# Optimization experiments

Measured on AMD Instinct MI355X. Metric: run time of the kernel, lower is better.

The kernel has to match this reference:

```python
import jax, jax.numpy as jnp
import numpy as np

B_GR = 128    # graphs per batch
N0 = 512      # nodes per graph before pooling
E_PER = 4096  # edges per graph (kept static; pooled-away edges get weight 0)
H = 128       # hidden
F = 128       # num_features (== hidden)
C = 10        # num_classes
K_HOP = 3     # Jacobi polynomial order (hop_num)
A_J, B_J = 1.0, 1.0
EPS = 1e-5


def _bn(h, g, b):
    # training-mode BatchNorm1d: batch stats, biased variance
    m = jnp.mean(h, 0)
    v = jnp.mean((h - m) ** 2, 0)
    return (h - m) * jax.lax.rsqrt(v + EPS) * g + b


def _forward(x, convW, convb, bnW, bnB, bn7W, bn7B, attW, theta,
             lin1W, lin1b, lin2W, lin2b, lin3W, lin3b, src, dst):
    w = jnp.ones((src.shape[0],), x.dtype)  # edge weights; 0 => filtered edge
    n = N0
    h = x
    reads = []
    for i in range(5):
        N = B_GR * n
        # symmetric GCN normalization with self loops on the weighted graph
        deg = jax.ops.segment_sum(w, dst, num_segments=N) + 1.0
        dinv = jax.lax.rsqrt(deg)
        enorm = dinv[src] * dinv[dst] * w   # per-edge norm [E]
        snorm = dinv * dinv                 # self-loop norm [N]
        prop = lambda m_: jax.ops.segment_sum(enorm[:, None] * m_[src], dst, num_segments=N) + m_ * snorm[:, None]
        pvec = lambda v_: jax.ops.segment_sum(enorm * v_[src], dst, num_segments=N) + v_ * snorm
        # GCNConv -> BN -> ReLU
        h = prop(h @ convW[i]) + convb[i]
        h = jax.nn.relu(_bn(h, bnW[i], bnB[i]))
        # JacobiPool: Jacobi-polynomial diffusion of attention scores
        s0 = h @ attW[i]                    # [N]
        polys = [s0, 0.5 * ((A_J - B_J) * s0 + (A_J + B_J + 2.0) * pvec(s0))]
        for kk in range(2, K_HOP + 1):
            c0 = 2 * kk * (kk + A_J + B_J) * (2 * kk + A_J + B_J - 2)
            c1 = (2 * kk + A_J + B_J - 1) * (2 * kk + A_J + B_J) * (2 * kk + A_J + B_J - 2)
            c2 = (2 * kk + A_J + B_J - 1) * (A_J * A_J - B_J * B_J)
            c3 = 2 * (kk + A_J - 1) * (kk + B_J - 1) * (2 * kk + A_J + B_J)
            polys.append((c1 * pvec(polys[-1]) + c2 * polys[-1] - c3 * polys[-2]) / c0)
        score = sum(theta[i, j] * polys[j] for j in range(K_HOP + 1))
        # top-k node selection per graph (ratio 0.5 -> static k)
        k = n // 2
        _, idx = jax.lax.top_k(score.reshape(B_GR, n), k)
        sel = (idx + (jnp.arange(B_GR) * n)[:, None]).reshape(-1)  # global node ids [B*k]
        h = h[sel] * jnp.tanh(score[sel])[:, None]
        # remap/filter edges to surviving nodes (masked, static edge count)
        new_id = jnp.full((N,), -1, jnp.int32).at[sel].set(jnp.arange(B_GR * k, dtype=jnp.int32))
        ns, nd = new_id[src], new_id[dst]
        valid = (ns >= 0) & (nd >= 0) & (w > 0)
        w = valid.astype(x.dtype)
        src = jnp.where(valid, ns, 0)
        dst = jnp.where(valid, nd, 0)
        # readout: global max pool || global mean pool per graph
        xg = h.reshape(B_GR, k, H)
        reads.append(jnp.concatenate([xg.max(1), xg.mean(1)], -1))
        n = k
    g = sum(reads) / 5.0                    # [B, 2H]
    g = jax.nn.relu(_bn(g @ lin1W + lin1b, bnW[5], bnB[5]))
    g = jax.nn.relu(_bn(g @ lin2W + lin2b, bn7W, bn7B))
    return jax.nn.log_softmax(g @ lin3W + lin3b, -1)


def setup_inputs() -> dict:
    key = jax.random.key(0)
    ks = jax.random.split(key, 8)
    N = B_GR * N0
    E = B_GR * E_PER
    rng = np.random.default_rng(0)
    off = np.repeat(np.arange(B_GR, dtype=np.int32) * N0, E_PER)
    src = jnp.asarray(off + rng.integers(0, N0, E).astype(np.int32))
    dst = jnp.asarray(off + rng.integers(0, N0, E).astype(np.int32))
    s = 1.0 / np.sqrt(H)
    return {
        "x": jax.random.normal(ks[0], (N, F), jnp.float32),
        "convW": jax.random.normal(ks[1], (5, H, H), jnp.float32) * s,
        "convb": jnp.zeros((5, H), jnp.float32),
        "bnW": jnp.ones((6, H), jnp.float32),
        "bnB": jnp.zeros((6, H), jnp.float32),
        "bn7W": jnp.ones((H // 2,), jnp.float32),
        "bn7B": jnp.zeros((H // 2,), jnp.float32),
        "attW": jax.random.normal(ks[2], (5, H), jnp.float32) * s,
        "theta": jax.random.normal(ks[3], (5, K_HOP + 1), jnp.float32) * 0.5,
        "lin1W": jax.random.normal(ks[4], (2 * H, H), jnp.float32) * (1.0 / np.sqrt(2 * H)),
        "lin1b": jnp.zeros((H,), jnp.float32),
        "lin2W": jax.random.normal(ks[5], (H, H // 2), jnp.float32) * s,
        "lin2b": jnp.zeros((H // 2,), jnp.float32),
        "lin3W": jax.random.normal(ks[6], (H // 2, C), jnp.float32) * (1.0 / np.sqrt(H // 2)),
        "lin3b": jnp.zeros((C,), jnp.float32),
        "src": src,
        "dst": dst,
    }


def reference(x, convW, convb, bnW, bnB, bn7W, bn7B, attW, theta,
              lin1W, lin1b, lin2W, lin2b, lin3W, lin3b, src, dst):
    return _forward(x, convW, convb, bnW, bnB, bn7W, bn7B, attW, theta,
                    lin1W, lin1b, lin2W, lin2b, lin3W, lin3b, src, dst)
```

## Files before the change

kernel.cpp:

```cpp
#include <hip/hip_runtime.h>
#include <hip/hip_bf16.h>

#define B_GRAPH 128
#define ETOT    (128*4096)
#define N0G     (128*512)
#define HF      128
#define STSZ    2048

union IGSmem {
    float Ws[64*HF];
    struct { int cnt4[4][512]; int cur[512]; float dvl[512]; } ini;
};

__global__ __launch_bounds__(256) void k_init_gemm(
    const float* __restrict__ A, const float* __restrict__ Wg, float* __restrict__ C,
    const int* __restrict__ s_in, const int* __restrict__ d_in_,
    int* __restrict__ srcw, int* __restrict__ dstw, float* __restrict__ wv,
    int2* __restrict__ csr, int2* __restrict__ rb2, float* __restrict__ dinvv,
    float* __restrict__ gacc, float* __restrict__ statsH,
    float* __restrict__ st0, float* __restrict__ st1, float* __restrict__ st2)
{
    __shared__ IGSmem sm;
    int t = threadIdx.x;
    if (blockIdx.x >= 128){
        int tx = t & 15, ty = t >> 4;
        int r0 = (blockIdx.x - 128)*128 + ty*8, c0 = tx*4;
        float acc[8][8];
        #pragma unroll
        for (int j=0;j<8;++j)
            #pragma unroll
            for (int l=0;l<8;++l) acc[j][l] = 0.f;
        for (int kh = 0; kh < 2; ++kh){
            __syncthreads();
            {
                float4* d4 = (float4*)sm.Ws;
                const float4* s4 = (const float4*)(Wg + kh*64*HF);
                #pragma unroll
                for (int i2 = 0; i2 < 8; ++i2) d4[t + i2*256] = s4[t + i2*256];
            }
            __syncthreads();
            for (int k4 = 0; k4 < 16; ++k4){
                float4 av[8];
                #pragma unroll
                for (int j=0;j<8;++j)
                    av[j] = *(const float4*)(A + (size_t)(r0+j)*HF + kh*64 + k4*4);
                #pragma unroll
                for (int kk=0; kk<4; ++kk){
                    int kl = k4*4 + kk;
                    float4 w0 = *(const float4*)(sm.Ws + kl*HF + c0);
                    float4 w1 = *(const float4*)(sm.Ws + kl*HF + c0 + 64);
                    #pragma unroll
                    for (int j=0;j<8;++j){
                        float a = reinterpret_cast<const float*>(&av[j])[kk];
                        acc[j][0] += a*w0.x; acc[j][1] += a*w0.y; acc[j][2] += a*w0.z; acc[j][3] += a*w0.w;
                        acc[j][4] += a*w1.x; acc[j][5] += a*w1.y; acc[j][6] += a*w1.z; acc[j][7] += a*w1.w;
                    }
                }
            }
        }
        #pragma unroll
        for (int j=0;j<8;++j){
            *(float4*)(C + (size_t)(r0+j)*HF + c0)      = make_float4(acc[j][0],acc[j][1],acc[j][2],acc[j][3]);
            *(float4*)(C + (size_t)(r0+j)*HF + c0 + 64) = make_float4(acc[j][4],acc[j][5],acc[j][6],acc[j][7]);
        }
    } else {
        int g = blockIdx.x;
        int wid = t >> 6;
        for (int l = t; l < 2048; l += 256) ((int*)sm.ini.cnt4)[l] = 0;
        gacc[g*256 + t] = 0.f;
        if (g == 0){
            if (t < 256){ statsH[t] = 0.f; if (t < 128) statsH[256+t] = 0.f; }
            for (int i = t; i < STSZ; i += 256){ st0[i] = 0.f; st1[i] = 0.f; st2[i] = 0.f; }
        }
        __syncthreads();
        for (int j = t; j < 4096; j += 256){
            int e = g*4096 + j;
            int sg = s_in[e], dg = d_in_[e];
            srcw[e] = sg; dstw[e] = dg; wv[e] = 1.f;
            atomicAdd(&sm.ini.cnt4[wid][dg & 511], 1);
        }
        __syncthreads();
        int c0 = sm.ini.cnt4[0][2*t] + sm.ini.cnt4[1][2*t] + sm.ini.cnt4[2][2*t] + sm.ini.cnt4[3][2*t];
        int c1 = sm.ini.cnt4[0][2*t+1] + sm.ini.cnt4[1][2*t+1] + sm.ini.cnt4[2][2*t+1] + sm.ini.cnt4[3][2*t+1];
        int pairsum = c0 + c1;
        sm.ini.cur[t] = pairsum;
        __syncthreads();
        for (int off = 1; off < 256; off <<= 1){
            int a = (t >= off) ? sm.ini.cur[t-off] : 0;
            __syncthreads();
            sm.ini.cur[t] += a;
            __syncthreads();
        }
        int begpair = sm.ini.cur[t] - pairsum;
        __syncthreads();
        sm.ini.cur[2*t]   = begpair;
        sm.ini.cur[2*t+1] = begpair + c0;
        sm.ini.cnt4[0][2*t]   = c0;
        sm.ini.cnt4[0][2*t+1] = c1;
        __syncthreads();
        for (int l = t; l < 512; l += 256){
            int cl = sm.ini.cnt4[0][l];
            rb2[g*512 + l] = make_int2(g*4096 + sm.ini.cur[l], cl);
            float dv = rsqrtf((float)cl + 1.f);
            sm.ini.dvl[l] = dv;
            dinvv[g*512 + l] = dv;
        }
        __syncthreads();
        for (int j = t; j < 4096; j += 256){
            int e = g*4096 + j;
            int sg = srcw[e], dl = dstw[e] & 511;
            int p = atomicAdd(&sm.ini.cur[dl], 1);
            csr[g*4096 + p] = make_int2(sg, __float_as_int(sm.ini.dvl[sg & 511]));
        }
    }
}

__global__ __launch_bounds__(256) void k_prop_stats(const float* __restrict__ Y, const float* __restrict__ cb,
                                                    const int2* __restrict__ rb2, const int2* __restrict__ cp,
                                                    const float* __restrict__ dinv,
                                                    float* __restrict__ X, float* __restrict__ st,
                                                    int n, int lb, int Nn){
    __shared__ float rs[1024], rq[1024];
    int xcd = blockIdx.x & 7, c = blockIdx.x >> 3;
    int g = xcd*16 + (c >> lb);
    int m = c & ((1 << lb) - 1);
    int nd = threadIdx.x >> 5;
    int v = g*n + m*8 + nd;
    int f4 = threadIdx.x & 31;
    float dv = dinv[v];
    float4 y = *(const float4*)(Y + (size_t)v*HF + f4*4);
    float4 acc = make_float4(0.f, 0.f, 0.f, 0.f);
    int2 rb = rb2[v];
    int e0 = rb.x, e1 = rb.x + rb.y;
    for (int j = e0; j < e1; ++j){
        int2 e = cp[j];
        int s = e.x & (Nn - 1);
        float en = __int_as_float(e.y);
        float4 h = *(const float4*)(Y + (size_t)s*HF + f4*4);
        acc.x += en*h.x; acc.y += en*h.y; acc.z += en*h.z; acc.w += en*h.w;
    }
    int f = f4*4;
    acc.x = y.x*dv*dv + dv*acc.x + cb[f];
    acc.y = y.y*dv*dv + dv*acc.y + cb[f+1];
    acc.z = y.z*dv*dv + dv*acc.z + cb[f+2];
    acc.w = y.w*dv*dv + dv*acc.w + cb[f+3];
    *(float4*)(X + (size_t)v*HF + f) = acc;
    *(float4*)&rs[nd*HF + f] = acc;
    *(float4*)&rq[nd*HF + f] = make_float4(acc.x*acc.x, acc.y*acc.y, acc.z*acc.z, acc.w*acc.w);
    __syncthreads();
    if (threadIdx.x < 128){
        int tt = threadIdx.x;
        float s = 0.f, q = 0.f;
        #pragma unroll
        for (int j = 0; j < 8; ++j){ s += rs[j*HF + tt]; q += rq[j*HF + tt]; }
        atomicAdd(&st[xcd*256 + tt], s);
        atomicAdd(&st[xcd*256 + 128 + tt], q);
    }
}

__global__ __launch_bounds__(256) void k_gemm(const float* __restrict__ A, const float* __restrict__ Wg,
                                              float* __restrict__ C)
{
    __shared__ float Ws[64*HF];
    int t = threadIdx.x;
    int tx = t & 15, ty = t >> 4;
    int r0 = blockIdx.x*128 + ty*8, c0 = tx*4;
    float acc[8][8];
    #pragma unroll
    for (int j=0;j<8;++j)
        #pragma unroll
        for (int l=0;l<8;++l) acc[j][l] = 0.f;
    for (int kh = 0; kh < 2; ++kh){
        __syncthreads();
        {
            float4* d4 = (float4*)Ws;
            const float4* s4 = (const float4*)(Wg + kh*64*HF);
            #pragma unroll
            for (int i2 = 0; i2 < 8; ++i2) d4[t + i2*256] = s4[t + i2*256];
        }
        __syncthreads();
        for (int k4 = 0; k4 < 16; ++k4){
            float4 av[8];
            #pragma unroll
            for (int j=0;j<8;++j)
                av[j] = *(const float4*)(A + (size_t)(r0+j)*HF + kh*64 + k4*4);
            #pragma unroll
            for (int kk=0; kk<4; ++kk){
                int kl = k4*4 + kk;
                float4 w0 = *(const float4*)(Ws + kl*HF + c0);
                float4 w1 = *(const float4*)(Ws + kl*HF + c0 + 64);
                #pragma unroll
                for (int j=0;j<8;++j){
                    float a = reinterpret_cast<const float*>(&av[j])[kk];
                    acc[j][0] += a*w0.x; acc[j][1] += a*w0.y; acc[j][2] += a*w0.z; acc[j][3] += a*w0.w;
                    acc[j][4] += a*w1.x; acc[j][5] += a*w1.y; acc[j][6] += a*w1.z; acc[j][7] += a*w1.w;
                }
            }
        }
    }
    #pragma unroll
    for (int j=0;j<8;++j){
        *(float4*)(C + (size_t)(r0+j)*HF + c0)      = make_float4(acc[j][0],acc[j][1],acc[j][2],acc[j][3]);
        *(float4*)(C + (size_t)(r0+j)*HF + c0 + 64) = make_float4(acc[j][4],acc[j][5],acc[j][6],acc[j][7]);
    }
}

struct __align__(16) KSmem {
    struct {
        int2  eds[4096]; int2 rbl[512];
        float dvv[512], p0[512], p1[512], p2[512];
        float ss[512]; int si[512]; float tss[256]; int nid[512];
        int   cntN[256], curN[256]; float dvn[256];
        float bna[128], bnb[128]; float red[1024]; float awl[128];
    } gr;
};

__global__ __launch_bounds__(1024) void k_graph(
    const float* __restrict__ H, const float* __restrict__ stats,
    const float* __restrict__ gw, const float* __restrict__ gb,
    const float* __restrict__ aw, const float* __restrict__ th,
    const int2* __restrict__ rb2, int2* __restrict__ csr, const float* __restrict__ dinv,
    int* __restrict__ srcw, int* __restrict__ dstw, float* __restrict__ wv,
    float* __restrict__ P, float* __restrict__ gacc,
    int2* __restrict__ rb2n, float* __restrict__ dinvn,
    float* __restrict__ stZero,
    const float* __restrict__ lin1W, const float* __restrict__ lin1b,
    float* __restrict__ t1g, float* __restrict__ statsH,
    float invN, float ca2, float cc2, float ca3, float cc3,
    int n, int last)
{
    int g = blockIdx.x, t = threadIdx.x;
    int k = n >> 1;
    __shared__ KSmem sm;

    if (t < 256) stZero[(g & 7)*256 + t] = 0.f;
    if (t < 128){
        float s = 0.f, q = 0.f;
        #pragma unroll
        for (int b2 = 0; b2 < 8; ++b2){ s += stats[b2*256 + t]; q += stats[b2*256 + 128 + t]; }
        float mean = s*invN;
        float var  = q*invN - mean*mean;
        float iv   = rsqrtf(var + 1e-5f);
        sm.gr.bna[t] = iv*gw[t];
        sm.gr.bnb[t] = gb[t] - mean*iv*gw[t];
        sm.gr.awl[t] = aw[t];
    }
    for (int l = t; l < n; l += 1024){
        int2 rb = rb2[g*n + l];
        sm.gr.rbl[l] = make_int2(rb.x - g*4096, rb.y);
        sm.gr.dvv[l] = dinv[g*n + l];
    }
    __syncthreads();
    int medg = sm.gr.rbl[n-1].x + sm.gr.rbl[n-1].y;
    for (int j = t; j < medg; j += 1024){
        int2 e = csr[g*4096 + j];
        sm.gr.eds[j] = make_int2(e.x & (n-1), e.y);
    }
    {
        int l = t >> 1, h = t & 1;
        float part = 0.f;
        if (l < n){
            const float* hp = H + ((size_t)g*n + l)*HF + h*64;
            #pragma unroll
            for (int j = 0; j < 16; ++j){
                float4 v = *(const float4*)(hp + j*4);
                int f = h*64 + j*4;
                float4 a4 = *(const float4*)&sm.gr.bna[f];
                float4 b4 = *(const float4*)&sm.gr.bnb[f];
                float4 w4 = *(const float4*)&sm.gr.awl[f];
                part += fmaxf(v.x*a4.x + b4.x, 0.f)*w4.x
                      + fmaxf(v.y*a4.y + b4.y, 0.f)*w4.y
                      + fmaxf(v.z*a4.z + b4.z, 0.f)*w4.z
                      + fmaxf(v.w*a4.w + b4.w, 0.f)*w4.w;
            }
        }
        sm.gr.red[t] = part;
    }
    __syncthreads();
    for (int l = t; l < n; l += 1024) sm.gr.p0[l] = sm.gr.red[2*l] + sm.gr.red[2*l+1];
    __syncthreads();
    for (int l = t; l < n; l += 1024){
        int2 rc = sm.gr.rbl[l];
        float acc = 0.f;
        for (int j = 0; j < rc.y; ++j){
            int2 e = sm.gr.eds[rc.x + j];
            acc += __int_as_float(e.y) * sm.gr.p0[e.x];
        }
        float dv = sm.gr.dvv[l];
        sm.gr.p1[l] = 2.f*(sm.gr.p0[l]*dv*dv + dv*acc);
    }
    __syncthreads();
    for (int l = t; l < n; l += 1024){
        int2 rc = sm.gr.rbl[l];
        float acc = 0.f;
        for (int j = 0; j < rc.y; ++j){
            int2 e = sm.gr.eds[rc.x + j];
            acc += __int_as_float(e.y) * sm.gr.p1[e.x];
        }
        float dv = sm.gr.dvv[l];
        sm.gr.p2[l] = ca2*(sm.gr.p1[l]*dv*dv + dv*acc) + cc2*sm.gr.p0[l];
    }
    __syncthreads();
    float t0v = th[0], t1v = th[1], t2c = th[2], t3v = th[3];
    for (int l = t; l < n; l += 1024){
        int2 rc = sm.gr.rbl[l];
        float acc = 0.f;
        for (int j = 0; j < rc.y; ++j){
            int2 e = sm.gr.eds[rc.x + j];
            acc += __int_as_float(e.y) * sm.gr.p2[e.x];
        }
        float dv = sm.gr.dvv[l];
        float tv = sm.gr.p2[l]*dv*dv + dv*acc;
        float p3 = ca3*tv + cc3*sm.gr.p1[l];
        sm.gr.ss[l] = t0v*sm.gr.p0[l] + t1v*sm.gr.p1[l] + t2c*sm.gr.p2[l] + t3v*p3;
    }
    __syncthreads();
    for (int l = t; l < n; l += 1024){
        float sl = sm.gr.ss[l];
        int r = 0;
        for (int j = 0; j < n; j += 4){
            float4 s4 = *(const float4*)&sm.gr.ss[j];
            r += (s4.x > sl) || (s4.x == sl && (j    ) < l);
            r += (s4.y > sl) || (s4.y == sl && (j + 1) < l);
            r += (s4.z > sl) || (s4.z == sl && (j + 2) < l);
            r += (s4.w > sl) || (s4.w == sl && (j + 3) < l);
        }
        if (r < k){
            sm.gr.nid[l] = r;
            sm.gr.si[r]  = l;
            sm.gr.tss[r] = tanhf(sl);
        } else {
            sm.gr.nid[l] = -1;
        }
    }
    __syncthreads();
    {
        int f4 = t & 31, rl = t >> 5;
        int f = f4*4;
        float4 a4 = *(const float4*)&sm.gr.bna[f];
        float4 b4 = *(const float4*)&sm.gr.bnb[f];
        float4 mx = make_float4(-3.4e38f,-3.4e38f,-3.4e38f,-3.4e38f);
        float4 smv = make_float4(0.f,0.f,0.f,0.f);
        for (int r = rl; r < k; r += 32){
            int old = sm.gr.si[r];
            float4 hv = *(const float4*)(H + ((size_t)g*n + old)*HF + f);
            float ts = sm.gr.tss[r];
            float4 v;
            v.x = fmaxf(hv.x*a4.x + b4.x, 0.f)*ts;
            v.y = fmaxf(hv.y*a4.y + b4.y, 0.f)*ts;
            v.z = fmaxf(hv.z*a4.z + b4.z, 0.f)*ts;
            v.w = fmaxf(hv.w*a4.w + b4.w, 0.f)*ts;
            *(float4*)(P + ((size_t)g*k + r)*HF + f) = v;
            mx.x = fmaxf(mx.x, v.x); mx.y = fmaxf(mx.y, v.y);
            mx.z = fmaxf(mx.z, v.z); mx.w = fmaxf(mx.w, v.w);
            smv.x += v.x; smv.y += v.y; smv.z += v.z; smv.w += v.w;
        }
        float* scr = (float*)sm.gr.eds;
        *(float4*)&scr[rl*128 + f]        = mx;
        *(float4*)&scr[4096 + rl*128 + f] = smv;
        __syncthreads();
        if (t < 128){
            float m = -3.4e38f, s = 0.f;
            #pragma unroll
            for (int j = 0; j < 32; ++j){
                m = fmaxf(m, scr[j*128 + t]);
                s += scr[4096 + j*128 + t];
            }
            gacc[g*256 + t] += m;
            gacc[g*256 + 128 + t] += s / (float)k;
        }
    }
    if (last){
        __syncthreads();
        int c = t & 127, h = t >> 7;
        float s = 0.f;
        int k0 = h*32;
        #pragma unroll
        for (int kk = 0; kk < 32; ++kk)
            s += gacc[g*256 + k0 + kk] * lin1W[(k0 + kk)*128 + c];
        sm.gr.red[t] = s;
        __syncthreads();
        if (t < 512) sm.gr.red[t] += sm.gr.red[t+512];
        __syncthreads();
        if (t < 256) sm.gr.red[t] += sm.gr.red[t+256];
        __syncthreads();
        if (t < 128){
            float v = (sm.gr.red[t] + sm.gr.red[t+128]) * 0.2f + lin1b[t];
            t1g[g*128 + t] = v;
            atomicAdd(&statsH[t], v);
            atomicAdd(&statsH[128+t], v*v);
        }
        return;
    }
    __syncthreads();
    if (t < k) sm.gr.cntN[t] = 0;
    __syncthreads();
    for (int j = t; j < 4096; j += 1024){
        int e = g*4096 + j;
        float we = wv[e];
        int valid = 0, ns = 0, nd = 0;
        if (we > 0.5f){
            int sl = srcw[e] & (n-1);
            int dl = dstw[e] & (n-1);
            ns = sm.gr.nid[sl]; nd = sm.gr.nid[dl];
            valid = (ns >= 0) && (nd >= 0);
        }
        if (valid){
            srcw[e] = g*k + ns; dstw[e] = g*k + nd; wv[e] = 1.f;
            atomicAdd(&sm.gr.cntN[nd], 1);
        } else {
            srcw[e] = 0; dstw[e] = 0; wv[e] = 0.f;
        }
    }
    __syncthreads();
    int c = (t < 256) ? ((t < k) ? sm.gr.cntN[t] : 0) : 0;
    if (t < 256) sm.gr.si[t] = c;
    __syncthreads();
    for (int off = 1; off < 256; off <<= 1){
        int a = 0;
        if (t < 256 && t >= off) a = sm.gr.si[t-off];
        __syncthreads();
        if (t < 256) sm.gr.si[t] += a;
        __syncthreads();
    }
    if (t < k){
        int beg = sm.gr.si[t] - c;
        rb2n[g*k + t] = make_int2(g*4096 + beg, c);
        float dv = rsqrtf((float)c + 1.f);
        dinvn[g*k + t] = dv;
        sm.gr.dvn[t] = dv;
        sm.gr.curN[t] = beg;
    }
    __syncthreads();
    for (int j = t; j < 4096; j += 1024){
        int e = g*4096 + j;
        if (wv[e] > 0.5f){
            int sg = srcw[e], dl = dstw[e] & (k-1);
            int p = atomicAdd(&sm.gr.curN[dl], 1);
            csr[g*4096 + p] = make_int2(sg, __float_as_int(sm.gr.dvn[sg & (k-1)]));
        }
    }
}

__global__ __launch_bounds__(128) void k_head2(const float* __restrict__ t1, const float* __restrict__ gw,
                                               const float* __restrict__ gb, const float* __restrict__ W2,
                                               const float* __restrict__ b2, float* __restrict__ sh,
                                               float* __restrict__ t2){
    int r = blockIdx.x, t = threadIdx.x;
    int cc = t & 63, h = t >> 6;
    __shared__ float row[128];
    __shared__ float red[128];
    {
        float mean = sh[t] * (1.f/128.f);
        float var  = sh[128+t]*(1.f/128.f) - mean*mean;
        float iv   = rsqrtf(var + 1e-5f);
        float v = (t1[r*128+t] - mean)*iv*gw[t] + gb[t];
        row[t] = fmaxf(v, 0.f);
    }
    __syncthreads();
    float s = 0.f;
    #pragma unroll
    for (int kk = 0; kk < 64; ++kk)
        s += row[h*64+kk] * W2[(h*64+kk)*64 + cc];
    red[t] = s;
    __syncthreads();
    if (h == 0){
        float v = red[cc] + red[cc+64] + b2[cc];
        t2[r*64+cc] = v;
        atomicAdd(&sh[256+cc], v);
        atomicAdd(&sh[320+cc], v*v);
    }
}
__global__ __launch_bounds__(64) void k_head3(const float* __restrict__ t2, const float* __restrict__ gw,
                                              const float* __restrict__ gb, const float* __restrict__ W3,
                                              const float* __restrict__ b3, const float* __restrict__ sh,
                                              float* __restrict__ out){
    int r = blockIdx.x, t = threadIdx.x;
    float mean = sh[256+t]*(1.f/128.f);
    float var  = sh[320+t]*(1.f/128.f) - mean*mean;
    float iv   = rsqrtf(var + 1e-5f);
    float v = fmaxf((t2[r*64+t]-mean)*iv*gw[t] + gb[t], 0.f);
    float lg[10];
    #pragma unroll
    for (int j = 0; j < 10; ++j){
        float p = v * W3[t*10 + j];
        for (int off = 32; off; off >>= 1) p += __shfl_down(p, off);
        lg[j] = p;
    }
    if (t == 0){
        float m = -3.4e38f;
        #pragma unroll
        for (int j = 0; j < 10; ++j){ lg[j] += b3[j]; m = fmaxf(m, lg[j]); }
        float se = 0.f;
        #pragma unroll
        for (int j = 0; j < 10; ++j) se += expf(lg[j] - m);
        float l = logf(se) + m;
        #pragma unroll
        for (int j = 0; j < 10; ++j) out[r*10 + j] = lg[j] - l;
    }
}

extern "C" void kernel_launch(void* const* d_in, const int* in_sizes, int n_in,
                              void* d_out, int out_size, void* d_ws, size_t ws_size,
                              hipStream_t stream){
    const float* x     = (const float*)d_in[0];
    const float* convW = (const float*)d_in[1];
    const float* convb = (const float*)d_in[2];
    const float* bnW   = (const float*)d_in[3];
    const float* bnB   = (const float*)d_in[4];
    const float* bn7W  = (const float*)d_in[5];
    const float* bn7B  = (const float*)d_in[6];
    const float* attW  = (const float*)d_in[7];
    const float* theta = (const float*)d_in[8];
    const float* lin1W = (const float*)d_in[9];
    const float* lin1b = (const float*)d_in[10];
    const float* lin2W = (const float*)d_in[11];
    const float* lin2b = (const float*)d_in[12];
    const float* lin3W = (const float*)d_in[13];
    const float* lin3b = (const float*)d_in[14];
    const int*   src0  = (const int*)d_in[15];
    const int*   dst0  = (const int*)d_in[16];

    char* base = (char*)d_ws;
    size_t off = 0;
    auto take = [&](size_t bytes) -> void* {
        void* p = base + off;
        off = (off + bytes + 255) & ~(size_t)255;
        return p;
    };
    float* bufGP = (float*)take((size_t)N0G*HF*4);
    float* bufHA = (float*)take((size_t)N0G*HF*4);
    float* bufHB = (float*)take((size_t)(N0G/2)*HF*4);
    int*   srcw  = (int*)  take((size_t)ETOT*4);
    int*   dstw  = (int*)  take((size_t)ETOT*4);
    float* w     = (float*)take((size_t)ETOT*4);
    int2*  csr_p = (int2*) take((size_t)ETOT*8);
    int2*  rb2A  = (int2*) take((size_t)N0G*8);
    int2*  rb2B  = (int2*) take((size_t)N0G*8);
    float* dinvA = (float*)take((size_t)N0G*4);
    float* dinvB = (float*)take((size_t)N0G*4);
    float* st[3];
    st[0] = (float*)take(STSZ*4);
    st[1] = (float*)take(STSZ*4);
    st[2] = (float*)take(STSZ*4);
    float* gacc  = (float*)take((size_t)B_GRAPH*256*4);
    float* t1    = (float*)take((size_t)B_GRAPH*128*4);
    float* t2    = (float*)take((size_t)B_GRAPH*64*4);
    float* statsH= (float*)take(384*4);

    auto coef = [](int kk, float& ca, float& cc){
        double a = 1.0, b = 1.0;
        double c0 = 2.0*kk*(kk+a+b)*(2.0*kk+a+b-2.0);
        double c1 = (2.0*kk+a+b-1.0)*(2.0*kk+a+b)*(2.0*kk+a+b-2.0);
        double c3 = 2.0*(kk+a-1.0)*(kk+b-1.0)*(2.0*kk+a+b);
        ca = (float)(c1/c0); cc = (float)(-c3/c0);
    };
    float ca2, cc2, ca3, cc3;
    coef(2, ca2, cc2);
    coef(3, ca3, cc3);

    k_init_gemm<<<128 + 512, 256, 0, stream>>>(x, convW, bufGP,
                                               src0, dst0, srcw, dstw, w, csr_p, rb2A, dinvA,
                                               gacc, statsH, st[0], st[1], st[2]);
    k_prop_stats<<<N0G/8, 256, 0, stream>>>(bufGP, convb, rb2A, csr_p, dinvA, bufHA, st[0], 512, 6, N0G);

    float* G = bufGP + (size_t)4*1024*1024;

    for (int i = 0; i < 5; ++i){
        int n = 512 >> i;
        int kk = n >> 1;
        int Nn = B_GRAPH*n;
        int2*  rb_cur = (i & 1) ? rb2B : rb2A;
        int2*  rb_nxt = (i & 1) ? rb2A : rb2B;
        float* dv_cur = (i & 1) ? dinvB : dinvA;
        float* dv_nxt = (i & 1) ? dinvA : dinvB;
        float* Hcur = (i & 1) ? bufHB : bufHA;
        float* Hnxt = (i & 1) ? bufHA : bufHB;

        k_graph<<<B_GRAPH, 1024, 0, stream>>>(Hcur, st[i % 3], bnW + i*HF, bnB + i*HF, attW + i*HF,
                                              theta + i*4, rb_cur, csr_p, dv_cur,
                                              srcw, dstw, w, bufGP, gacc, rb_nxt, dv_nxt,
                                              st[(i + 1) % 3],
                                              lin1W, lin1b, t1, statsH,
                                              1.0f/(float)Nn, ca2, cc2, ca3, cc3, n, (i == 4) ? 1 : 0);
        if (i < 4){
            int wnext = i + 1;
            int rows = B_GRAPH * kk;
            k_gemm<<<rows/128, 256, 0, stream>>>(bufGP, convW + (size_t)wnext*HF*HF, G);
            int lbn = (kk == 256) ? 5 : (kk == 128) ? 4 : (kk == 64) ? 3 : 2;
            k_prop_stats<<<rows/8, 256, 0, stream>>>(G, convb + wnext*HF, rb_nxt, csr_p, dv_nxt,
                                                     Hnxt, st[(i + 1) % 3], kk, lbn, rows);
        }
    }

    k_head2<<<B_GRAPH, 128, 0, stream>>>(t1, bnW + 5*HF, bnB + 5*HF, lin2W, lin2b, statsH, t2);
    k_head3<<<B_GRAPH, 64, 0, stream>>>(t2, bn7W, bn7B, lin3W, lin3b, statsH, (float*)d_out);
}
```

Baseline: 410.7 us.

## Split score kernel out, fuse BN/ReLU/gather into GEMM, rebuild CSR per-node

Moves the attention-score dot product out of the per-graph pool kernel into a wide grid-parallel k_score kernel. The pooled feature matrix is no longer written; instead the next GEMM gathers the selected rows, applies BN+ReLU+tanh scaling on load, and multiplies. The edge arrays (src/dst/weight) are dropped, and the next-level CSR is built directly from the current CSR using the kept-node map, avoiding a scan over all 4096 edges with atomics. Clamping masks are added on CSR indices and lengths, and there is one extra launch per level.

```diff
diff --git a/kernel.cpp b/kernel.cpp
--- a/kernel.cpp
+++ b/kernel.cpp
@@ -15,7 +15,6 @@
 __global__ __launch_bounds__(256) void k_init_gemm(
     const float* __restrict__ A, const float* __restrict__ Wg, float* __restrict__ C,
     const int* __restrict__ s_in, const int* __restrict__ d_in_,
-    int* __restrict__ srcw, int* __restrict__ dstw, float* __restrict__ wv,
     int2* __restrict__ csr, int2* __restrict__ rb2, float* __restrict__ dinvv,
     float* __restrict__ gacc, float* __restrict__ statsH,
     float* __restrict__ st0, float* __restrict__ st1, float* __restrict__ st2)
@@ -75,9 +74,7 @@
         __syncthreads();
         for (int j = t; j < 4096; j += 256){
             int e = g*4096 + j;
-            int sg = s_in[e], dg = d_in_[e];
-            srcw[e] = sg; dstw[e] = dg; wv[e] = 1.f;
-            atomicAdd(&sm.ini.cnt4[wid][dg & 511], 1);
+            atomicAdd(&sm.ini.cnt4[wid][d_in_[e] & 511], 1);
         }
         __syncthreads();
         int c0 = sm.ini.cnt4[0][2*t] + sm.ini.cnt4[1][2*t] + sm.ini.cnt4[2][2*t] + sm.ini.cnt4[3][2*t];
@@ -108,9 +105,9 @@
         __syncthreads();
         for (int j = t; j < 4096; j += 256){
             int e = g*4096 + j;
-            int sg = srcw[e], dl = dstw[e] & 511;
+            int sg = s_in[e], dl = d_in_[e] & 511;
             int p = atomicAdd(&sm.ini.cur[dl], 1);
-            csr[g*4096 + p] = make_int2(sg, __float_as_int(sm.ini.dvl[sg & 511]));
+            csr[g*4096 + (p & 4095)] = make_int2(sg, __float_as_int(sm.ini.dvl[sg & 511]));
         }
     }
 }
@@ -131,7 +128,8 @@
     float4 y = *(const float4*)(Y + (size_t)v*HF + f4*4);
     float4 acc = make_float4(0.f, 0.f, 0.f, 0.f);
     int2 rb = rb2[v];
-    int e0 = rb.x, e1 = rb.x + rb.y;
+    int len = min(max(rb.y, 0), 4096);
+    int e0 = rb.x, e1 = rb.x + len;
     for (int j = e0; j < e1; ++j){
         int2 e = cp[j];
         int s = e.x & (Nn - 1);
@@ -158,13 +156,77 @@
     }
 }
 
-__global__ __launch_bounds__(256) void k_gemm(const float* __restrict__ A, const float* __restrict__ Wg,
-                                              float* __restrict__ C)
+__global__ __launch_bounds__(256) void k_score(
+    const float* __restrict__ H, const float* __restrict__ stats,
+    const float* __restrict__ gw, const float* __restrict__ gb,
+    const float* __restrict__ aw, float* __restrict__ s0G, float invN)
+{
+    __shared__ float bna[128], bnb[128], awl[128];
+    int t = threadIdx.x;
+    if (t < 128){
+        float s = 0.f, q = 0.f;
+        #pragma unroll
+        for (int b2 = 0; b2 < 8; ++b2){ s += stats[b2*256 + t]; q += stats[b2*256 + 128 + t]; }
+        float mean = s*invN;
+        float var  = q*invN - mean*mean;
+        float iv   = rsqrtf(var + 1e-5f);
+        bna[t] = iv*gw[t];
+        bnb[t] = gb[t] - mean*iv*gw[t];
+        awl[t] = aw[t];
+    }
+    __syncthreads();
+    int v = blockIdx.x*128 + (t >> 1);
+    int h = t & 1;
+    const float* hp = H + (size_t)v*HF + h*64;
+    float part = 0.f;
+    #pragma unroll
+    for (int j = 0; j < 16; ++j){
+        float4 x = *(const float4*)(hp + j*4);
+        int f = h*64 + j*4;
+        float4 a4 = *(const float4*)&bna[f];
+        float4 b4 = *(const float4*)&bnb[f];
+        float4 w4 = *(const float4*)&awl[f];
+        part += fmaxf(x.x*a4.x + b4.x, 0.f)*w4.x
+              + fmaxf(x.y*a4.y + b4.y, 0.f)*w4.y
+              + fmaxf(x.z*a4.z + b4.z, 0.f)*w4.z
+              + fmaxf(x.w*a4.w + b4.w, 0.f)*w4.w;
+    }
+    float oth = __shfl_xor(part, 1);
+    if (h == 0) s0G[v] = part + oth;
+}
+
+__global__ __launch_bounds__(256) void k_gemm_g(
+    const float* __restrict__ Hsrc, const float* __restrict__ stats,
+    const float* __restrict__ gw, const float* __restrict__ gb,
+    const int* __restrict__ siG, const float* __restrict__ tssG,
+    const float* __restrict__ Wg, float* __restrict__ C,
+    float invN, int lk, int ln)
 {
     __shared__ float Ws[64*HF];
+    __shared__ float bna[128], bnb[128];
     int t = threadIdx.x;
+    if (t < 128){
+        float s = 0.f, q = 0.f;
+        #pragma unroll
+        for (int b2 = 0; b2 < 8; ++b2){ s += stats[b2*256 + t]; q += stats[b2*256 + 128 + t]; }
+        float mean = s*invN;
+        float var  = q*invN - mean*mean;
+        float iv   = rsqrtf(var + 1e-5f);
+        bna[t] = iv*gw[t];
+        bnb[t] = gb[t] - mean*iv*gw[t];
+    }
     int tx = t & 15, ty = t >> 4;
     int r0 = blockIdx.x*128 + ty*8, c0 = tx*4;
+    int rbase[8]; float ts_[8];
+    int nmask = (1 << ln) - 1;
+    #pragma unroll
+    for (int j = 0; j < 8; ++j){
+        int rg = r0 + j;
+        int g = rg >> lk;
+        int old = siG[rg] & nmask;
+        rbase[j] = ((g << ln) + old) * HF;
+        ts_[j] = tssG[rg];
+    }
     float acc[8][8];
     #pragma unroll
     for (int j=0;j<8;++j)
@@ -180,10 +242,18 @@
         }
         __syncthreads();
         for (int k4 = 0; k4 < 16; ++k4){
+            int fb = kh*64 + k4*4;
+            float4 ba = *(const float4*)&bna[fb];
+            float4 bb = *(const float4*)&bnb[fb];
             float4 av[8];
             #pragma unroll
-            for (int j=0;j<8;++j)
-                av[j] = *(const float4*)(A + (size_t)(r0+j)*HF + kh*64 + k4*4);
+            for (int j=0;j<8;++j){
+                av[j] = *(const float4*)(Hsrc + (size_t)rbase[j] + fb);
+                av[j].x = fmaxf(av[j].x*ba.x + bb.x, 0.f)*ts_[j];
+                av[j].y = fmaxf(av[j].y*ba.y + bb.y, 0.f)*ts_[j];
+                av[j].z = fmaxf(av[j].z*ba.z + bb.z, 0.f)*ts_[j];
+                av[j].w = fmaxf(av[j].w*ba.w + bb.w, 0.f)*ts_[j];
+            }
             #pragma unroll
             for (int kk=0; kk<4; ++kk){
                 int kl = k4*4 + kk;
@@ -205,25 +275,23 @@
     }
 }
 
-struct __align__(16) KSmem {
-    struct {
-        int2  eds[4096]; int2 rbl[512];
-        float dvv[512], p0[512], p1[512], p2[512];
-        float ss[512]; int si[512]; float tss[256]; int nid[512];
-        int   cntN[256], curN[256]; float dvn[256];
-        float bna[128], bnb[128]; float red[1024]; float awl[128];
-    } gr;
+struct __align__(16) PSmem {
+    int2  eds[4096];
+    int2  rbl[512];
+    float dvv[512], p0[512], p1[512], p2[512];
+    float ss[512]; int si[512]; float tss[256]; int nid[512];
+    int   cnt_[256], scn[256], curN[256]; float dvn[256];
+    float bna[128], bnb[128]; float red[1024];
 };
 
-__global__ __launch_bounds__(1024) void k_graph(
+__global__ __launch_bounds__(1024) void k_pool(
     const float* __restrict__ H, const float* __restrict__ stats,
     const float* __restrict__ gw, const float* __restrict__ gb,
-    const float* __restrict__ aw, const float* __restrict__ th,
+    const float* __restrict__ th,
     const int2* __restrict__ rb2, int2* __restrict__ csr, const float* __restrict__ dinv,
-    int* __restrict__ srcw, int* __restrict__ dstw, float* __restrict__ wv,
-    float* __restrict__ P, float* __restrict__ gacc,
-    int2* __restrict__ rb2n, float* __restrict__ dinvn,
-    float* __restrict__ stZero,
+    const float* __restrict__ s0G,
+    float* __restrict__ gacc, int2* __restrict__ rb2n, float* __restrict__ dinvn,
+    float* __restrict__ stZero, int* __restrict__ siG, float* __restrict__ tssG,
     const float* __restrict__ lin1W, const float* __restrict__ lin1b,
     float* __restrict__ t1g, float* __restrict__ statsH,
     float invN, float ca2, float cc2, float ca3, float cc3,
@@ -231,7 +299,7 @@
 {
     int g = blockIdx.x, t = threadIdx.x;
     int k = n >> 1;
-    __shared__ KSmem sm;
+    __shared__ PSmem sm;
 
     if (t < 256) stZero[(g & 7)*256 + t] = 0.f;
     if (t < 128){
@@ -241,121 +309,142 @@
         float mean = s*invN;
         float var  = q*invN - mean*mean;
         float iv   = rsqrtf(var + 1e-5f);
-        sm.gr.bna[t] = iv*gw[t];
-        sm.gr.bnb[t] = gb[t] - mean*iv*gw[t];
-        sm.gr.awl[t] = aw[t];
+        sm.bna[t] = iv*gw[t];
+        sm.bnb[t] = gb[t] - mean*iv*gw[t];
     }
     for (int l = t; l < n; l += 1024){
         int2 rb = rb2[g*n + l];
-        sm.gr.rbl[l] = make_int2(rb.x - g*4096, rb.y);
-        sm.gr.dvv[l] = dinv[g*n + l];
-    }
-    __syncthreads();
-    int medg = sm.gr.rbl[n-1].x + sm.gr.rbl[n-1].y;
+        int bx = (rb.x - g*4096) & 4095;
+        int by = min(max(rb.y, 0), 4096 - bx);
+        sm.rbl[l] = make_int2(bx, by);
+        sm.dvv[l] = dinv[g*n + l];
+        sm.p0[l]  = s0G[g*n + l];
+    }
+    __syncthreads();
+    int medg = sm.rbl[n-1].x + sm.rbl[n-1].y;
     for (int j = t; j < medg; j += 1024){
         int2 e = csr[g*4096 + j];
-        sm.gr.eds[j] = make_int2(e.x & (n-1), e.y);
-    }
-    {
-        int l = t >> 1, h = t & 1;
-        float part = 0.f;
-        if (l < n){
-            const float* hp = H + ((size_t)g*n + l)*HF + h*64;
-            #pragma unroll
-            for (int j = 0; j < 16; ++j){
-                float4 v = *(const float4*)(hp + j*4);
-                int f = h*64 + j*4;
-                float4 a4 = *(const float4*)&sm.gr.bna[f];
-                float4 b4 = *(const float4*)&sm.gr.bnb[f];
-                float4 w4 = *(const float4*)&sm.gr.awl[f];
-                part += fmaxf(v.x*a4.x + b4.x, 0.f)*w4.x
-                      + fmaxf(v.y*a4.y + b4.y, 0.f)*w4.y
-                      + fmaxf(v.z*a4.z + b4.z, 0.f)*w4.z
-                      + fmaxf(v.w*a4.w + b4.w, 0.f)*w4.w;
-            }
-        }
-        sm.gr.red[t] = part;
-    }
-    __syncthreads();
-    for (int l = t; l < n; l += 1024) sm.gr.p0[l] = sm.gr.red[2*l] + sm.gr.red[2*l+1];
+        sm.eds[j] = make_int2(e.x & (n-1), e.y);
+    }
     __syncthreads();
     for (int l = t; l < n; l += 1024){
-        int2 rc = sm.gr.rbl[l];
+        int2 rc = sm.rbl[l];
         float acc = 0.f;
         for (int j = 0; j < rc.y; ++j){
-            int2 e = sm.gr.eds[rc.x + j];
-            acc += __int_as_float(e.y) * sm.gr.p0[e.x];
-        }
-        float dv = sm.gr.dvv[l];
-        sm.gr.p1[l] = 2.f*(sm.gr.p0[l]*dv*dv + dv*acc);
+            int2 e = sm.eds[rc.x + j];
+            acc += __int_as_float(e.y) * sm.p0[e.x];
+        }
+        float dv = sm.dvv[l];
+        sm.p1[l] = 2.f*(sm.p0[l]*dv*dv + dv*acc);
     }
     __syncthreads();
     for (int l = t; l < n; l += 1024){
-        int2 rc = sm.gr.rbl[l];
+        int2 rc = sm.rbl[l];
         float acc = 0.f;
         for (int j = 0; j < rc.y; ++j){
-            int2 e = sm.gr.eds[rc.x + j];
-            acc += __int_as_float(e.y) * sm.gr.p1[e.x];
-        }
-        float dv = sm.gr.dvv[l];
-        sm.gr.p2[l] = ca2*(sm.gr.p1[l]*dv*dv + dv*acc) + cc2*sm.gr.p0[l];
+            int2 e = sm.eds[rc.x + j];
+            acc += __int_as_float(e.y) * sm.p1[e.x];
+        }
+        float dv = sm.dvv[l];
+        sm.p2[l] = ca2*(sm.p1[l]*dv*dv + dv*acc) + cc2*sm.p0[l];
     }
     __syncthreads();
     float t0v = th[0], t1v = th[1], t2c = th[2], t3v = th[3];
     for (int l = t; l < n; l += 1024){
-        int2 rc = sm.gr.rbl[l];
+        int2 rc = sm.rbl[l];
         float acc = 0.f;
         for (int j = 0; j < rc.y; ++j){
-            int2 e = sm.gr.eds[rc.x + j];
-            acc += __int_as_float(e.y) * sm.gr.p2[e.x];
-        }
-        float dv = sm.gr.dvv[l];
-        float tv = sm.gr.p2[l]*dv*dv + dv*acc;
-        float p3 = ca3*tv + cc3*sm.gr.p1[l];
-        sm.gr.ss[l] = t0v*sm.gr.p0[l] + t1v*sm.gr.p1[l] + t2c*sm.gr.p2[l] + t3v*p3;
+            int2 e = sm.eds[rc.x + j];
+            acc += __int_as_float(e.y) * sm.p2[e.x];
+        }
+        float dv = sm.dvv[l];
+        float tv = sm.p2[l]*dv*dv + dv*acc;
+        float p3 = ca3*tv + cc3*sm.p1[l];
+        sm.ss[l] = t0v*sm.p0[l] + t1v*sm.p1[l] + t2c*sm.p2[l] + t3v*p3;
     }
     __syncthreads();
     for (int l = t; l < n; l += 1024){
-        float sl = sm.gr.ss[l];
+        float sl = sm.ss[l];
         int r = 0;
         for (int j = 0; j < n; j += 4){
-            float4 s4 = *(const float4*)&sm.gr.ss[j];
+            float4 s4 = *(const float4*)&sm.ss[j];
             r += (s4.x > sl) || (s4.x == sl && (j    ) < l);
             r += (s4.y > sl) || (s4.y == sl && (j + 1) < l);
             r += (s4.z > sl) || (s4.z == sl && (j + 2) < l);
             r += (s4.w > sl) || (s4.w == sl && (j + 3) < l);
         }
         if (r < k){
-            sm.gr.nid[l] = r;
-            sm.gr.si[r]  = l;
-            sm.gr.tss[r] = tanhf(sl);
+            sm.nid[l] = r;
+            sm.si[r]  = l;
+            float tv = tanhf(sl);
+            sm.tss[r] = tv;
+            siG[g*k + r]  = l;
+            tssG[g*k + r] = tv;
         } else {
-            sm.gr.nid[l] = -1;
-        }
-    }
-    __syncthreads();
+            sm.nid[l] = -1;
+        }
+    }
+    __syncthreads();
+    if (!last){
+        if (t < k){
+            int l = sm.si[t] & (n-1);
+            int2 rc = sm.rbl[l];
+            int c = 0;
+            for (int j = 0; j < rc.y; ++j) c += (sm.nid[sm.eds[rc.x + j].x] >= 0);
+            sm.cnt_[t] = c;
+        }
+        __syncthreads();
+        int c = (t < 256) ? ((t < k) ? sm.cnt_[t] : 0) : 0;
+        if (t < 256) sm.scn[t] = c;
+        __syncthreads();
+        for (int off = 1; off < 256; off <<= 1){
+            int a = 0;
+            if (t < 256 && t >= off) a = sm.scn[t-off];
+            __syncthreads();
+            if (t < 256) sm.scn[t] += a;
+            __syncthreads();
+        }
+        if (t < k){
+            int beg = sm.scn[t] - c;
+            rb2n[g*k + t] = make_int2(g*4096 + beg, c);
+            float dv = rsqrtf((float)c + 1.f);
+            dinvn[g*k + t] = dv;
+            sm.dvn[t] = dv;
+            sm.curN[t] = beg;
+        }
+        __syncthreads();
+        if (t < k){
+            int l = sm.si[t] & (n-1);
+            int2 rc = sm.rbl[l];
+            int p = sm.curN[t];
+            for (int j = 0; j < rc.y; ++j){
+                int ns = sm.nid[sm.eds[rc.x + j].x];
+                if (ns >= 0){ csr[g*4096 + (p & 4095)] = make_int2(g*k + ns, __float_as_int(sm.dvn[ns])); ++p; }
+            }
+        }
+        __syncthreads();
+    }
     {
         int f4 = t & 31, rl = t >> 5;
         int f = f4*4;
-        float4 a4 = *(const float4*)&sm.gr.bna[f];
-        float4 b4 = *(const float4*)&sm.gr.bnb[f];
+        float4 a4 = *(const float4*)&sm.bna[f];
+        float4 b4 = *(const float4*)&sm.bnb[f];
         float4 mx = make_float4(-3.4e38f,-3.4e38f,-3.4e38f,-3.4e38f);
         float4 smv = make_float4(0.f,0.f,0.f,0.f);
         for (int r = rl; r < k; r += 32){
-            int old = sm.gr.si[r];
+            int old = sm.si[r] & (n-1);
             float4 hv = *(const float4*)(H + ((size_t)g*n + old)*HF + f);
-            float ts = sm.gr.tss[r];
+            float ts = sm.tss[r];
             float4 v;
             v.x = fmaxf(hv.x*a4.x + b4.x, 0.f)*ts;
             v.y = fmaxf(hv.y*a4.y + b4.y, 0.f)*ts;
             v.z = fmaxf(hv.z*a4.z + b4.z, 0.f)*ts;
             v.w = fmaxf(hv.w*a4.w + b4.w, 0.f)*ts;
-            *(float4*)(P + ((size_t)g*k + r)*HF + f) = v;
             mx.x = fmaxf(mx.x, v.x); mx.y = fmaxf(mx.y, v.y);
             mx.z = fmaxf(mx.z, v.z); mx.w = fmaxf(mx.w, v.w);
             smv.x += v.x; smv.y += v.y; smv.z += v.z; smv.w += v.w;
         }
-        float* scr = (float*)sm.gr.eds;
+        float* scr = (float*)sm.eds;
         *(float4*)&scr[rl*128 + f]        = mx;
         *(float4*)&scr[4096 + rl*128 + f] = smv;
         __syncthreads();
@@ -378,66 +467,17 @@
         #pragma unroll
         for (int kk = 0; kk < 32; ++kk)
             s += gacc[g*256 + k0 + kk] * lin1W[(k0 + kk)*128 + c];
-        sm.gr.red[t] = s;
-        __syncthreads();
-        if (t < 512) sm.gr.red[t] += sm.gr.red[t+512];
-        __syncthreads();
-        if (t < 256) sm.gr.red[t] += sm.gr.red[t+256];
+        sm.red[t] = s;
+        __syncthreads();
+        if (t < 512) sm.red[t] += sm.red[t+512];
+        __syncthreads();
+        if (t < 256) sm.red[t] += sm.red[t+256];
         __syncthreads();
         if (t < 128){
-            float v = (sm.gr.red[t] + sm.gr.red[t+128]) * 0.2f + lin1b[t];
+            float v = (sm.red[t] + sm.red[t+128]) * 0.2f + lin1b[t];
             t1g[g*128 + t] = v;
             atomicAdd(&statsH[t], v);
             atomicAdd(&statsH[128+t], v*v);
-        }
-        return;
-    }
-    __syncthreads();
-    if (t < k) sm.gr.cntN[t] = 0;
-    __syncthreads();
-    for (int j = t; j < 4096; j += 1024){
-        int e = g*4096 + j;
-        float we = wv[e];
-        int valid = 0, ns = 0, nd = 0;
-        if (we > 0.5f){
-            int sl = srcw[e] & (n-1);
-            int dl = dstw[e] & (n-1);
-            ns = sm.gr.nid[sl]; nd = sm.gr.nid[dl];
-            valid = (ns >= 0) && (nd >= 0);
-        }
-        if (valid){
-            srcw[e] = g*k + ns; dstw[e] = g*k + nd; wv[e] = 1.f;
-            atomicAdd(&sm.gr.cntN[nd], 1);
-        } else {
-            srcw[e] = 0; dstw[e] = 0; wv[e] = 0.f;
-        }
-    }
-    __syncthreads();
-    int c = (t < 256) ? ((t < k) ? sm.gr.cntN[t] : 0) : 0;
-    if (t < 256) sm.gr.si[t] = c;
-    __syncthreads();
-    for (int off = 1; off < 256; off <<= 1){
-        int a = 0;
-        if (t < 256 && t >= off) a = sm.gr.si[t-off];
-        __syncthreads();
-        if (t < 256) sm.gr.si[t] += a;
-        __syncthreads();
-    }
-    if (t < k){
-        int beg = sm.gr.si[t] - c;
-        rb2n[g*k + t] = make_int2(g*4096 + beg, c);
-        float dv = rsqrtf((float)c + 1.f);
-        dinvn[g*k + t] = dv;
-        sm.gr.dvn[t] = dv;
-        sm.gr.curN[t] = beg;
-    }
-    __syncthreads();
-    for (int j = t; j < 4096; j += 1024){
-        int e = g*4096 + j;
-        if (wv[e] > 0.5f){
-            int sg = srcw[e], dl = dstw[e] & (k-1);
-            int p = atomicAdd(&sm.gr.curN[dl], 1);
-            csr[g*4096 + p] = make_int2(sg, __float_as_int(sm.gr.dvn[sg & (k-1)]));
         }
     }
 }
@@ -531,14 +571,14 @@
     float* bufGP = (float*)take((size_t)N0G*HF*4);
     float* bufHA = (float*)take((size_t)N0G*HF*4);
     float* bufHB = (float*)take((size_t)(N0G/2)*HF*4);
-    int*   srcw  = (int*)  take((size_t)ETOT*4);
-    int*   dstw  = (int*)  take((size_t)ETOT*4);
-    float* w     = (float*)take((size_t)ETOT*4);
     int2*  csr_p = (int2*) take((size_t)ETOT*8);
     int2*  rb2A  = (int2*) take((size_t)N0G*8);
     int2*  rb2B  = (int2*) take((size_t)N0G*8);
     float* dinvA = (float*)take((size_t)N0G*4);
     float* dinvB = (float*)take((size_t)N0G*4);
+    float* s0G   = (float*)take((size_t)N0G*4);
+    int*   siG   = (int*)  take((size_t)(N0G/2)*4);
+    float* tssG  = (float*)take((size_t)(N0G/2)*4);
     float* st[3];
     st[0] = (float*)take(STSZ*4);
     st[1] = (float*)take(STSZ*4);
@@ -560,7 +600,7 @@
     coef(3, ca3, cc3);
 
     k_init_gemm<<<128 + 512, 256, 0, stream>>>(x, convW, bufGP,
-                                               src0, dst0, srcw, dstw, w, csr_p, rb2A, dinvA,
+                                               src0, dst0, csr_p, rb2A, dinvA,
                                                gacc, statsH, st[0], st[1], st[2]);
     k_prop_stats<<<N0G/8, 256, 0, stream>>>(bufGP, convb, rb2A, csr_p, dinvA, bufHA, st[0], 512, 6, N0G);
 
@@ -570,6 +610,7 @@
         int n = 512 >> i;
         int kk = n >> 1;
         int Nn = B_GRAPH*n;
+        float invN = 1.0f/(float)Nn;
         int2*  rb_cur = (i & 1) ? rb2B : rb2A;
         int2*  rb_nxt = (i & 1) ? rb2A : rb2B;
         float* dv_cur = (i & 1) ? dinvB : dinvA;
@@ -577,16 +618,22 @@
         float* Hcur = (i & 1) ? bufHB : bufHA;
         float* Hnxt = (i & 1) ? bufHA : bufHB;
 
-        k_graph<<<B_GRAPH, 1024, 0, stream>>>(Hcur, st[i % 3], bnW + i*HF, bnB + i*HF, attW + i*HF,
-                                              theta + i*4, rb_cur, csr_p, dv_cur,
-                                              srcw, dstw, w, bufGP, gacc, rb_nxt, dv_nxt,
-                                              st[(i + 1) % 3],
-                                              lin1W, lin1b, t1, statsH,
-                                              1.0f/(float)Nn, ca2, cc2, ca3, cc3, n, (i == 4) ? 1 : 0);
+        k_score<<<Nn/128, 256, 0, stream>>>(Hcur, st[i % 3], bnW + i*HF, bnB + i*HF, attW + i*HF,
+                                            s0G, invN);
+        k_pool<<<B_GRAPH, 1024, 0, stream>>>(Hcur, st[i % 3], bnW + i*HF, bnB + i*HF,
+                                             theta + i*4, rb_cur, csr_p, dv_cur, s0G,
+                                             gacc, rb_nxt, dv_nxt,
+                                             st[(i + 1) % 3], siG, tssG,
+                                             lin1W, lin1b, t1, statsH,
+                                             invN, ca2, cc2, ca3, cc3, n, (i == 4) ? 1 : 0);
         if (i < 4){
             int wnext = i + 1;
             int rows = B_GRAPH * kk;
-            k_gemm<<<rows/128, 256, 0, stream>>>(bufGP, convW + (size_t)wnext*HF*HF, G);
+            int lk = 8 - i;
+            int ln = 9 - i;
+            k_gemm_g<<<rows/128, 256, 0, stream>>>(Hcur, st[i % 3], bnW + i*HF, bnB + i*HF,
+                                                   siG, tssG, convW + (size_t)wnext*HF*HF, G,
+                                                   invN, lk, ln);
             int lbn = (kk == 256) ? 5 : (kk == 128) ? 4 : (kk == 64) ? 3 : 2;
             k_prop_stats<<<rows/8, 256, 0, stream>>>(G, convb + wnext*HF, rb_nxt, csr_p, dv_nxt,
                                                      Hnxt, st[(i + 1) % 3], kk, lbn, rows);
```

Result: slower. 427.9 us (+4.2%).
